# Kernel tuning notes

Hardware: AMD Instinct MI355X
Metric: run time of the kernel (lower is better)

Reference implementation:

```python
import jax, jax.numpy as jnp
import numpy as np
import math

HIDDEN = 2048
NUM_HEADS = 16
HEAD_DIM = HIDDEN // NUM_HEADS  # 128
B, S = 2, 2048


def setup_inputs() -> dict:
    key = jax.random.key(0)
    ks = jax.random.split(key, 10)
    std = 1.0 / math.sqrt(HIDDEN)
    x = jax.random.normal(ks[0], (B, S, HIDDEN), dtype=jnp.float32)
    # causal mask, broadcastable to [B, H, S, S]; 0 entries get masked
    attention_mask = jnp.tril(jnp.ones((S, S), dtype=jnp.int32))[None, None, :, :]
    qw_w = jax.random.normal(ks[1], (HIDDEN, HIDDEN), dtype=jnp.float32) * std
    qw_b = jax.random.normal(ks[2], (HIDDEN,), dtype=jnp.float32) * std
    kw_w = jax.random.normal(ks[3], (HEAD_DIM, HIDDEN), dtype=jnp.float32) * std
    kw_b = jax.random.normal(ks[4], (HEAD_DIM,), dtype=jnp.float32) * std
    vw_w = jax.random.normal(ks[5], (HEAD_DIM, HIDDEN), dtype=jnp.float32) * std
    vw_b = jax.random.normal(ks[6], (HEAD_DIM,), dtype=jnp.float32) * std
    ow_w = jax.random.normal(ks[7], (HIDDEN, HIDDEN), dtype=jnp.float32) * std
    ow_b = jax.random.normal(ks[8], (HIDDEN,), dtype=jnp.float32) * std
    return dict(x=x, attention_mask=attention_mask, qw_w=qw_w, qw_b=qw_b,
                kw_w=kw_w, kw_b=kw_b, vw_w=vw_w, vw_b=vw_b, ow_w=ow_w, ow_b=ow_b)


def reference(x, attention_mask, qw_w, qw_b, kw_w, kw_b, vw_w, vw_b, ow_w, ow_b):
    b, s, _ = x.shape
    # projections (torch Linear: x @ W.T + b)
    qx = x @ qw_w.T + qw_b                      # [B, S, H*D]
    kx = x @ kw_w.T + kw_b                      # [B, S, D] (single KV head)
    vx = x @ vw_w.T + vw_b                      # [B, S, D]
    q = jnp.swapaxes(qx.reshape(b, s, NUM_HEADS, HEAD_DIM), 1, 2)  # [B, H, S, D]
    scale = 1.0 / math.sqrt(HEAD_DIM)
    scores = jnp.einsum('bhqd,bkd->bhqk', q, kx) * scale           # [B, H, S, S]
    scores = jnp.where(attention_mask == 0, jnp.float32(-9e15), scores)
    probs = jax.nn.softmax(scores, axis=-1)
    aw = jnp.einsum('bhqk,bkd->bhqd', probs, vx)                   # [B, H, S, D]
    # faithful to original: transpose(-1,-2) then view(B, -1, H*D)
    aw = jnp.swapaxes(aw, -1, -2).reshape(b, -1, NUM_HEADS * HEAD_DIM)  # [B, S, H*D]
    return aw @ ow_w.T + ow_b
```

## Files before the change

kernel.cpp:

```cpp
#include <hip/hip_runtime.h>
#include <stdint.h>

#define HIDDEN 2048
#define NHEADS 16
#define HDIM 128
#define BATCH 2
#define SEQ 2048
#define MTOT (BATCH*SEQ)
#define PW 2304

typedef __attribute__((ext_vector_type(4))) float f32x4;
typedef __attribute__((ext_vector_type(8))) short s16x8;
typedef __attribute__((ext_vector_type(4))) short s16x4;

static __device__ __forceinline__ unsigned short f2bf(float f) {
  unsigned u = __float_as_uint(f);
  u += 0x7fff + ((u >> 16) & 1);
  return (unsigned short)(u >> 16);
}

static __device__ __forceinline__ unsigned cvtpk(float a, float b) {
  unsigned r;
  asm("v_cvt_pk_bf16_f32 %0, %1, %2" : "=v"(r) : "v"(a), "v"(b));
  return r;
}

static __device__ __forceinline__ f32x4 mfma32(s16x8 a, s16x8 b, f32x4 c) {
  return __builtin_amdgcn_mfma_f32_16x16x32_bf16(a, b, c, 0, 0, 0);
}
static __device__ __forceinline__ f32x4 mfma16(s16x4 a, s16x4 b, f32x4 c) {
  return __builtin_amdgcn_mfma_f32_16x16x16bf16_1k(a, b, c, 0, 0, 0);
}

static __device__ __forceinline__ void gload16(const unsigned short* g, unsigned short* l) {
  __builtin_amdgcn_global_load_lds(
      (const __attribute__((address_space(1))) void*)g,
      (__attribute__((address_space(3))) void*)l, 16, 0, 0);
}

static __device__ __forceinline__ void cast4(const float* __restrict__ in, int ii,
                                             unsigned short* __restrict__ out) {
  float4 v = reinterpret_cast<const float4*>(in)[ii];
  ushort4 o;
  o.x = f2bf(v.x); o.y = f2bf(v.y); o.z = f2bf(v.z); o.w = f2bf(v.w);
  reinterpret_cast<ushort4*>(out)[ii] = o;
}

__global__ void cast_f32_to_bf16(const float* __restrict__ in,
                                 unsigned short* __restrict__ out, int n4) {
  int i = blockIdx.x * blockDim.x + threadIdx.x;
  if (i >= n4) return;
  cast4(in, i, out);
}

__global__ void cast_all(const float* __restrict__ x,  const float* __restrict__ qw,
                         const float* __restrict__ kw, const float* __restrict__ vw,
                         const float* __restrict__ qb, const float* __restrict__ kb,
                         const float* __restrict__ vb,
                         unsigned short* __restrict__ xb,
                         unsigned short* __restrict__ wqkv,
                         float* __restrict__ bqkv) {
  int i = blockIdx.x * 256 + threadIdx.x;
  if (i < 2097152)      cast4(x,  i,           xb);
  else if (i < 3145728) cast4(qw, i - 2097152, wqkv);
  else if (i < 3211264) cast4(kw, i - 3145728, wqkv + 4194304);
  else if (i < 3276800) cast4(vw, i - 3211264, wqkv + 4456448);
  else {
    int k = i - 3276800;
    if (k < 2304)
      bqkv[k] = (k < 2048) ? qb[k] : (k < 2176) ? kb[k - 2048] : vb[k - 2176];
  }
}

template<bool OUT_BF16, bool QKV>
__global__ __launch_bounds__(256) void gemm_lds(
    const unsigned short* __restrict__ A, const unsigned short* __restrict__ B,
    const float* __restrict__ bias, void* __restrict__ Cout,
    unsigned short* __restrict__ Kp, unsigned short* __restrict__ Vp,
    int M, int N, int K)
{
  __shared__ unsigned short lsA[2][128 * 64];
  __shared__ unsigned short lsB[2][128 * 64];
  const int tid  = threadIdx.x;
  const int lane = tid & 63, wid = tid >> 6;
  const int g = lane >> 4, lr = lane & 15;
  const int m0 = blockIdx.x * 128, n0 = blockIdx.y * 128;
  const int wm = (wid >> 1) * 64,  wn = (wid & 1) * 64;
  f32x4 acc[4][4] = {};

  const int srow = tid >> 3;
  const int scol = ((tid & 7) ^ (srow & 7)) * 8;
  const unsigned short* gA = A + (size_t)(m0 + srow) * K + scol;
  const unsigned short* gB = B + (size_t)(n0 + srow) * K + scol;

  auto stage = [&](int k0, int buf) {
#pragma unroll
    for (int i = 0; i < 4; ++i) {
      gload16(gA + k0 + (size_t)(i * 32) * K, lsA[buf] + wid * 512 + i * 2048);
      gload16(gB + k0 + (size_t)(i * 32) * K, lsB[buf] + wid * 512 + i * 2048);
    }
  };

  stage(0, 0);
  __syncthreads();

  int cur = 0;
  for (int k0 = 0; k0 < K; k0 += 64) {
    if (k0 + 64 < K) stage(k0 + 64, cur ^ 1);
#pragma unroll
    for (int kk = 0; kk < 2; ++kk) {
      s16x8 a[4], b[4];
#pragma unroll
      for (int i = 0; i < 4; ++i) {
        const int row = wm + i * 16 + lr;
        a[i] = *reinterpret_cast<const s16x8*>(
            &lsA[cur][row * 64 + (((kk * 4 + g) ^ (row & 7)) * 8)]);
      }
#pragma unroll
      for (int j = 0; j < 4; ++j) {
        const int row = wn + j * 16 + lr;
        b[j] = *reinterpret_cast<const s16x8*>(
            &lsB[cur][row * 64 + (((kk * 4 + g) ^ (row & 7)) * 8)]);
      }
#pragma unroll
      for (int i = 0; i < 4; ++i)
#pragma unroll
        for (int j = 0; j < 4; ++j)
          acc[i][j] = mfma32(a[i], b[j], acc[i][j]);
    }
    __syncthreads();
    cur ^= 1;
  }

  if (QKV && n0 == 2048) {
#pragma unroll
    for (int i = 0; i < 4; ++i)
#pragma unroll
      for (int j = 0; j < 4; ++j) {
        const int col = n0 + wn + j * 16 + lr;
        const int d   = col - 2048;
        const float bv = bias[col];
        const int c2 = d >> 5, gk = (d >> 3) & 3, e = d & 7;
        const int row0 = m0 + wm + i * 16 + g * 4;
#pragma unroll
        for (int r = 0; r < 4; ++r) {
          const int s  = row0 + r;
          const int bb = s >> 11, sl = s & 2047;
          Kp[(size_t)bb * 262144 + (size_t)(sl >> 4) * 2048 + c2 * 512
             + gk * 128 + (sl & 15) * 8 + e] = f2bf(acc[i][j][r] + bv);
        }
      }
    return;
  }
  if (QKV && n0 == 2176) {
#pragma unroll
    for (int i = 0; i < 4; ++i)
#pragma unroll
      for (int j = 0; j < 4; ++j) {
        const int col = n0 + wn + j * 16 + lr;
        const float bv = bias[col];
        const int row0 = m0 + wm + i * 16 + g * 4;
        const int bb = row0 >> 11, sl = row0 & 2047;
        s16x4 ov;
#pragma unroll
        for (int r = 0; r < 4; ++r) ov[r] = (short)f2bf(acc[i][j][r] + bv);
        *reinterpret_cast<s16x4*>(
            &Vp[(size_t)bb * 262144 + (size_t)(sl >> 2) * 512 + (col - 2176) * 4]) = ov;
      }
    return;
  }
#pragma unroll
  for (int i = 0; i < 4; ++i)
#pragma unroll
    for (int j = 0; j < 4; ++j) {
      const int col  = n0 + wn + j * 16 + lr;
      const float bv = bias[col];
      const int row0 = m0 + wm + i * 16 + g * 4;
#pragma unroll
      for (int r = 0; r < 4; ++r) {
        float v = acc[i][j][r] + bv;
        if (QKV) {
          const float QS = 0.08838834764831845f * 1.4426950408889634f;
          reinterpret_cast<unsigned short*>(Cout)[(size_t)(row0 + r) * 2048 + col] =
              f2bf(v * QS);
        } else if (OUT_BF16)
          reinterpret_cast<unsigned short*>(Cout)[(size_t)(row0 + r) * N + col] = f2bf(v);
        else
          reinterpret_cast<float*>(Cout)[(size_t)(row0 + r) * N + col] = v;
      }
    }
}

__global__ __launch_bounds__(256, 3) void mqa_attn(
    const unsigned short* __restrict__ qx,
    const unsigned short* __restrict__ Kp,
    const unsigned short* __restrict__ Vp,
    unsigned short* __restrict__ OT)
{
  __shared__ unsigned int accL[4][2][16][66];
  __shared__ float lmL[4][2][16][2];

  const int bx = blockIdx.x;
  const int qtile = 63 - (bx >> 5);
  const int hb = bx & 31;
  const int h  = hb & 15, b = hb >> 4;

  const int tid = threadIdx.x;
  const int lane = tid & 63, wid = tid >> 6;
  const int g = lane >> 4, lr = lane & 15;
  const int q0 = qtile * 32;
  const float THR2 = 11.541560327111708f;

  const unsigned short* Kpb = Kp + (size_t)b * 262144;
  const unsigned short* Vpb = Vp + (size_t)b * 262144;

  s16x8 qf[2][4];
  int qglob[2], dt[2];
#pragma unroll
  for (int s = 0; s < 2; ++s) {
    qglob[s] = q0 + s * 16 + lr;
    dt[s]    = qtile * 2 + s;
    const unsigned short* Qb =
        qx + (size_t)(b * SEQ + q0 + s * 16 + lr) * 2048 + h * HDIM;
#pragma unroll
    for (int c = 0; c < 4; ++c)
      qf[s][c] = *reinterpret_cast<const s16x8*>(Qb + c * 32 + g * 8);
  }

  float m[2] = {-1e30f, -1e30f}, lsum[2] = {0.f, 0.f};
  f32x4 acc[2][8] = {};

  const int jmax = qtile * 2 + 1;
  for (int j = wid; j <= jmax; j += 4) {
    const int k0 = j * 16;
    s16x8 kf[4];
#pragma unroll
    for (int c = 0; c < 4; ++c)
      kf[c] = *reinterpret_cast<const s16x8*>(
          Kpb + ((size_t)(j * 4 + c) * 64 + lane) * 8);
    const unsigned short* vrow = Vpb + ((size_t)(k0 >> 2) + g) * 512;
    s16x4 vf8[8];
#pragma unroll
    for (int t = 0; t < 8; ++t)
      vf8[t] = *reinterpret_cast<const s16x4*>(&vrow[(t * 16 + lr) * 4]);

    s16x4 pb[2];
#pragma unroll
    for (int s = 0; s < 2; ++s) {
      if (j > dt[s]) {
        pb[s] = (s16x4){0, 0, 0, 0};
        continue;
      }
      f32x4 sc = {0.f, 0.f, 0.f, 0.f};
#pragma unroll
      for (int c = 0; c < 4; ++c) sc = mfma32(kf[c], qf[s][c], sc);
      float sv[4];
      if (j == dt[s]) {
#pragma unroll
        for (int r = 0; r < 4; ++r) {
          const int kv = k0 + g * 4 + r;
          sv[r] = (kv <= qglob[s]) ? sc[r] : -1e30f;
        }
      } else {
#pragma unroll
        for (int r = 0; r < 4; ++r) sv[r] = sc[r];
      }
      const float tmax = fmaxf(fmaxf(sv[0], sv[1]), fmaxf(sv[2], sv[3]));
      if (__any(tmax > m[s] + THR2)) {
        float rmax = fmaxf(tmax, __shfl_xor(tmax, 16));
        rmax = fmaxf(rmax, __shfl_xor(rmax, 32));
        const float mnew  = fmaxf(m[s], rmax);
        const float alpha = exp2f(m[s] - mnew);
        lsum[s] *= alpha;
#pragma unroll
        for (int t = 0; t < 8; ++t)
#pragma unroll
          for (int r = 0; r < 4; ++r) acc[s][t][r] *= alpha;
        m[s] = mnew;
      }
      float p[4];
#pragma unroll
      for (int r = 0; r < 4; ++r) p[r] = exp2f(sv[r] - m[s]);
      lsum[s] += (p[0] + p[1]) + (p[2] + p[3]);
      union { s16x4 v4; unsigned u[2]; } pk;
      pk.u[0] = cvtpk(p[0], p[1]);
      pk.u[1] = cvtpk(p[2], p[3]);
      pb[s] = pk.v4;
    }
#pragma unroll
    for (int t = 0; t < 8; ++t) {
      acc[0][t] = mfma16(vf8[t], pb[0], acc[0][t]);
      acc[1][t] = mfma16(vf8[t], pb[1], acc[1][t]);
    }
  }

#pragma unroll
  for (int s = 0; s < 2; ++s) {
    float t = lsum[s];
    t += __shfl_xor(t, 16);
    t += __shfl_xor(t, 32);
    lsum[s] = t;
  }

  if (g == 0) {
#pragma unroll
    for (int s = 0; s < 2; ++s) {
      lmL[wid][s][lr][0] = m[s];
      lmL[wid][s][lr][1] = lsum[s];
    }
  }
#pragma unroll
  for (int s = 0; s < 2; ++s)
#pragma unroll
    for (int t = 0; t < 8; ++t) {
      accL[wid][s][lr][t * 8 + g * 2]     = cvtpk(acc[s][t][0], acc[s][t][1]);
      accL[wid][s][lr][t * 8 + g * 2 + 1] = cvtpk(acc[s][t][2], acc[s][t][3]);
    }
  __syncthreads();

  const int q  = tid & 31, grp = tid >> 5;
  const int ms = q >> 4,  mlr = q & 15;
  float mv[4], lv[4], M = -1e30f;
#pragma unroll
  for (int v = 0; v < 4; ++v) {
    mv[v] = lmL[v][ms][mlr][0];
    lv[v] = lmL[v][ms][mlr][1];
    M = fmaxf(M, mv[v]);
  }
  float L = 0.f, w[4];
#pragma unroll
  for (int v = 0; v < 4; ++v) { w[v] = exp2f(mv[v] - M); L += w[v] * lv[v]; }
  float o[16] = {};
#pragma unroll
  for (int v = 0; v < 4; ++v) {
#pragma unroll
    for (int u = 0; u < 8; ++u) {
      const unsigned pw = accL[v][ms][mlr][grp * 8 + u];
      o[2 * u]     += w[v] * __uint_as_float(pw << 16);
      o[2 * u + 1] += w[v] * __uint_as_float(pw & 0xffff0000u);
    }
  }
  const float inv = 1.0f / L;
  const size_t obase = ((size_t)b * HIDDEN + h * HDIM + grp * 16) * SEQ + q0 + q;
#pragma unroll
  for (int e = 0; e < 16; ++e)
    OT[obase + (size_t)e * SEQ] = f2bf(o[e] * inv);
}

extern "C" void kernel_launch(void* const* d_in, const int* in_sizes, int n_in,
                              void* d_out, int out_size, void* d_ws, size_t ws_size,
                              hipStream_t stream) {
  (void)in_sizes; (void)n_in; (void)out_size;
  const float* x    = (const float*)d_in[0];
  const float* qw_w = (const float*)d_in[2];
  const float* qw_b = (const float*)d_in[3];
  const float* kw_w = (const float*)d_in[4];
  const float* kw_b = (const float*)d_in[5];
  const float* vw_w = (const float*)d_in[6];
  const float* vw_b = (const float*)d_in[7];
  const float* ow_w = (const float*)d_in[8];
  const float* ow_b = (const float*)d_in[9];
  float* out = (float*)d_out;

  if (ws_size < 26223616) return;
  char* ob = (char*)d_out;
  char* ws = (char*)d_ws;
  unsigned short* xb   = (unsigned short*)(ws);
  unsigned short* wqkv = (unsigned short*)(ws + 16777216);
  float*          bqkv = (float*)        (ws + 26214400);
  unsigned short* owb  = (unsigned short*)(ws);
  unsigned short* awT  = (unsigned short*)(ws + 8388608);
  unsigned short* qx   = (unsigned short*)(ob);
  unsigned short* kpb  = (unsigned short*)(ob + 16777216);
  unsigned short* vpb  = (unsigned short*)(ob + 17825792);

  cast_all<<<12809, 256, 0, stream>>>(x, qw_w, kw_w, vw_w, qw_b, kw_b, vw_b,
                                      xb, wqkv, bqkv);

  gemm_lds<true , true ><<<dim3(32, 18), 256, 0, stream>>>(xb, wqkv, bqkv, qx, kpb, vpb, MTOT, PW, HIDDEN);

  cast_f32_to_bf16<<<4096, 256, 0, stream>>>(ow_w, owb, 1048576);

  mqa_attn<<<2048, 256, 0, stream>>>(qx, kpb, vpb, awT);

  gemm_lds<false, false><<<dim3(32, 16), 256, 0, stream>>>(awT, owb, ow_b, out, nullptr, nullptr, MTOT, HIDDEN, HIDDEN);
}
```

Baseline: 195.5 us.

## Fold K/V projection columns into Q GEMM blocks to remove extra grid columns

The fused QKV GEMM previously launched 18 column tiles, two of which handled the 256 K/V output columns. Each of the 16 Q column tiles now also stages a 16-row slice of the K/V weights into an extra LDS buffer. It accumulates that slice with four extra MFMAs per k-step and writes it to the packed K or V layout in the epilogue. This shrinks the grid from 576 to 512 blocks to cut tail-wave quantization, at the cost of more per-block work and duplicated K/V MFMAs across the paired waves.

```diff
diff --git a/kernel.cpp b/kernel.cpp
--- a/kernel.cpp
+++ b/kernel.cpp
@@ -81,17 +81,23 @@
 {
   __shared__ unsigned short lsA[2][128 * 64];
   __shared__ unsigned short lsB[2][128 * 64];
+  __shared__ unsigned short lsC[2][16 * 64];
   const int tid  = threadIdx.x;
   const int lane = tid & 63, wid = tid >> 6;
   const int g = lane >> 4, lr = lane & 15;
   const int m0 = blockIdx.x * 128, n0 = blockIdx.y * 128;
+  const int by = blockIdx.y;
   const int wm = (wid >> 1) * 64,  wn = (wid & 1) * 64;
   f32x4 acc[4][4] = {};
+  f32x4 acc_kv[4] = {};
 
   const int srow = tid >> 3;
   const int scol = ((tid & 7) ^ (srow & 7)) * 8;
   const unsigned short* gA = A + (size_t)(m0 + srow) * K + scol;
   const unsigned short* gB = B + (size_t)(n0 + srow) * K + scol;
+  const int crow = (wid & 1) * 8 + (lane >> 3);
+  const unsigned short* gC = B + (size_t)(2048 + by * 16 + crow) * K
+                               + (((lane & 7) ^ (lane >> 3)) * 8);
 
   auto stage = [&](int k0, int buf) {
 #pragma unroll
@@ -99,6 +105,8 @@
       gload16(gA + k0 + (size_t)(i * 32) * K, lsA[buf] + wid * 512 + i * 2048);
       gload16(gB + k0 + (size_t)(i * 32) * K, lsB[buf] + wid * 512 + i * 2048);
     }
+    if (QKV && wid < 2)
+      gload16(gC + k0, lsC[buf] + wid * 512);
   };
 
   stage(0, 0);
@@ -127,46 +135,61 @@
 #pragma unroll
         for (int j = 0; j < 4; ++j)
           acc[i][j] = mfma32(a[i], b[j], acc[i][j]);
+      if (QKV) {
+        s16x8 bc = *reinterpret_cast<const s16x8*>(
+            &lsC[cur][lr * 64 + (((kk * 4 + g) ^ (lr & 7)) * 8)]);
+#pragma unroll
+        for (int i = 0; i < 4; ++i)
+          acc_kv[i] = mfma32(a[i], bc, acc_kv[i]);
+      }
     }
     __syncthreads();
     cur ^= 1;
   }
 
-  if (QKV && n0 == 2048) {
+  if (QKV) {
 #pragma unroll
     for (int i = 0; i < 4; ++i)
 #pragma unroll
       for (int j = 0; j < 4; ++j) {
-        const int col = n0 + wn + j * 16 + lr;
-        const int d   = col - 2048;
+        const int col  = n0 + wn + j * 16 + lr;
         const float bv = bias[col];
-        const int c2 = d >> 5, gk = (d >> 3) & 3, e = d & 7;
+        const int row0 = m0 + wm + i * 16 + g * 4;
+        const float QS = 0.08838834764831845f * 1.4426950408889634f;
+#pragma unroll
+        for (int r = 0; r < 4; ++r)
+          reinterpret_cast<unsigned short*>(Cout)[(size_t)(row0 + r) * 2048 + col] =
+              f2bf((acc[i][j][r] + bv) * QS);
+      }
+    const int colg = by * 16 + lr;
+    const float bv = bias[2048 + colg];
+    if (colg < 128) {
+      const int d  = colg;
+      const int c2 = d >> 5, gk = (d >> 3) & 3, e = d & 7;
+#pragma unroll
+      for (int i = 0; i < 4; ++i) {
         const int row0 = m0 + wm + i * 16 + g * 4;
 #pragma unroll
         for (int r = 0; r < 4; ++r) {
           const int s  = row0 + r;
           const int bb = s >> 11, sl = s & 2047;
           Kp[(size_t)bb * 262144 + (size_t)(sl >> 4) * 2048 + c2 * 512
-             + gk * 128 + (sl & 15) * 8 + e] = f2bf(acc[i][j][r] + bv);
+             + gk * 128 + (sl & 15) * 8 + e] = f2bf(acc_kv[i][r] + bv);
         }
       }
-    return;
-  }
-  if (QKV && n0 == 2176) {
-#pragma unroll
-    for (int i = 0; i < 4; ++i)
-#pragma unroll
-      for (int j = 0; j < 4; ++j) {
-        const int col = n0 + wn + j * 16 + lr;
-        const float bv = bias[col];
+    } else {
+      const int d = colg - 128;
+#pragma unroll
+      for (int i = 0; i < 4; ++i) {
         const int row0 = m0 + wm + i * 16 + g * 4;
         const int bb = row0 >> 11, sl = row0 & 2047;
         s16x4 ov;
 #pragma unroll
-        for (int r = 0; r < 4; ++r) ov[r] = (short)f2bf(acc[i][j][r] + bv);
+        for (int r = 0; r < 4; ++r) ov[r] = (short)f2bf(acc_kv[i][r] + bv);
         *reinterpret_cast<s16x4*>(
-            &Vp[(size_t)bb * 262144 + (size_t)(sl >> 2) * 512 + (col - 2176) * 4]) = ov;
-      }
+            &Vp[(size_t)bb * 262144 + (size_t)(sl >> 2) * 512 + d * 4]) = ov;
+      }
+    }
     return;
   }
 #pragma unroll
@@ -179,11 +202,7 @@
 #pragma unroll
       for (int r = 0; r < 4; ++r) {
         float v = acc[i][j][r] + bv;
-        if (QKV) {
-          const float QS = 0.08838834764831845f * 1.4426950408889634f;
-          reinterpret_cast<unsigned short*>(Cout)[(size_t)(row0 + r) * 2048 + col] =
-              f2bf(v * QS);
-        } else if (OUT_BF16)
+        if (OUT_BF16)
           reinterpret_cast<unsigned short*>(Cout)[(size_t)(row0 + r) * N + col] = f2bf(v);
         else
           reinterpret_cast<float*>(Cout)[(size_t)(row0 + r) * N + col] = v;
@@ -377,7 +396,7 @@
   cast_all<<<12809, 256, 0, stream>>>(x, qw_w, kw_w, vw_w, qw_b, kw_b, vw_b,
                                       xb, wqkv, bqkv);
 
-  gemm_lds<true , true ><<<dim3(32, 18), 256, 0, stream>>>(xb, wqkv, bqkv, qx, kpb, vpb, MTOT, PW, HIDDEN);
+  gemm_lds<true , true ><<<dim3(32, 16), 256, 0, stream>>>(xb, wqkv, bqkv, qx, kpb, vpb, MTOT, PW, HIDDEN);
 
   cast_f32_to_bf16<<<4096, 256, 0, stream>>>(ow_w, owb, 1048576);
 
```

New measurement: 169.5 us. -13.3%, faster.
